# Kernel optimization log

Measured on AMD Instinct MI355X. Metric: run time of the kernel, lower is better.

The kernel has to match this reference:

```python
import jax, jax.numpy as jnp
import numpy as np

EMB = 768

def _mlp2(x, Wa, Wb):
    # relu(LL2(relu(LL1(x)))), bias-free linears stored as [out, in]
    return jax.nn.relu(jax.nn.relu(x @ Wa.T) @ Wb.T)

def setup_inputs() -> dict:
    key = jax.random.key(0)
    ks = jax.random.split(key, 6)
    n, m = 16, 4096  # maxlen = 64 paragraphs -> 64*64 pair slots
    X_data = jax.random.normal(ks[0], (n, 1 + m, 3 * EMB), dtype=jnp.float32)
    # first token carries num_clusters metadata (unused by the differentiable path)
    W1 = jax.random.normal(ks[1], (256, EMB), dtype=jnp.float32) * 0.02
    W2 = jax.random.normal(ks[2], (128, 256), dtype=jnp.float32) * 0.02
    W3 = jax.random.normal(ks[3], (256, EMB), dtype=jnp.float32) * 0.02
    W4 = jax.random.normal(ks[4], (128, 256), dtype=jnp.float32) * 0.02
    W5 = jax.random.normal(ks[5], (1, 128), dtype=jnp.float32) * 0.02
    return {"X_data": X_data, "W1": W1, "W2": W2, "W3": W3, "W4": W4, "W5": W5}

def reference(X_data, W1, W2, W3, W4, W5):
    # CATSCluster differentiable path: QueryScaler on X_data[:, 1:, :]
    X = X_data[:, 1:, :]                      # [n, m, 3*EMB]
    Xq = X[..., :EMB]
    Xp1 = X[..., EMB:2 * EMB]
    Xp2 = X[..., 2 * EMB:]
    Xp1z = _mlp2(Xp1, W1, W2)                 # [n, m, 128]
    Xp2z = _mlp2(Xp2, W1, W2)
    Xqz = _mlp2(Xq, W3, W4)
    Xpqz = Xqz * jnp.abs(Xp1z - Xp2z)         # [n, m, 128]
    dist = jnp.tanh(jax.nn.relu(Xpqz @ W5.T))[..., 0]  # [n, m]
    n, m = dist.shape
    p = int(np.sqrt(m))                       # maxlen
    # batch_pairscore_matrix fed to the host-side clustering step
    return dist.reshape(n, p, p)
```

## Files before the change

kernel.cpp:

```cpp
#include <hip/hip_runtime.h>
#include <hip/hip_bf16.h>


typedef short short8 __attribute__((ext_vector_type(8)));
typedef float f32x4 __attribute__((ext_vector_type(4)));

#define W1H_OFF 0u
#define W1L_OFF 196608u
#define W3H_OFF 393216u
#define W3L_OFF 589824u
#define W2H_OFF 786432u
#define W2L_OFF 819200u
#define W4H_OFF 851968u
#define W4L_OFF 884736u

__device__ __forceinline__ unsigned short bf16_rne(float f) {
  unsigned int u = __float_as_uint(f);
  u += 0x7FFFu + ((u >> 16) & 1u);
  return (unsigned short)(u >> 16);
}

__device__ __forceinline__ void split_bf16(float f, unsigned short& h, unsigned short& l) {
  h = bf16_rne(f);
  float fh = __uint_as_float(((unsigned int)h) << 16);
  l = bf16_rne(f - fh);
}

__global__ __launch_bounds__(256) void prep_weights(
    const float* __restrict__ W1, const float* __restrict__ W2,
    const float* __restrict__ W3, const float* __restrict__ W4,
    unsigned short* __restrict__ ws)
{
  int i = blockIdx.x * 256 + threadIdx.x;
  if (i < 196608) {
    unsigned short h, l;
    split_bf16(W1[i], h, l); ws[W1H_OFF + i] = h; ws[W1L_OFF + i] = l;
    split_bf16(W3[i], h, l); ws[W3H_OFF + i] = h; ws[W3L_OFF + i] = l;
    if (i < 32768) {
      split_bf16(W2[i], h, l); ws[W2H_OFF + i] = h; ws[W2L_OFF + i] = l;
      split_bf16(W4[i], h, l); ws[W4H_OFF + i] = h; ws[W4L_OFF + i] = l;
    }
  }
}

#define STRIDE_A 40
#define STRIDE_H 264

__global__ __launch_bounds__(256) void catsc_main(
    const float* __restrict__ X, const unsigned short* __restrict__ ws,
    const float* __restrict__ W5, float* __restrict__ out)
{
  __shared__ short lsA[2][2][64 * STRIDE_A];
  __shared__ short lsH[64 * STRIDE_H];
  __shared__ float lsPart[4][64];

  const int tid  = threadIdx.x;
  const int wave = tid >> 6;
  const int lane = tid & 63;
  const int l15  = lane & 15;
  const int q    = lane >> 4;
  const int blk  = blockIdx.x;

  const float* Xb = X + (size_t)((blk >> 6) * 4097 + 1 + ((blk & 63) << 6)) * 2304;

  const int srow = tid >> 3;
  const int f4   = (tid & 7) << 2;

  f32x4 z[3][4][2];

#pragma unroll
  for (int s = 0; s < 3; ++s) {
    const unsigned short* B1h = ws + (s == 0 ? W3H_OFF : W1H_OFF);
    const unsigned short* B1l = ws + (s == 0 ? W3L_OFF : W1L_OFF);
    const unsigned short* B2h = ws + (s == 0 ? W4H_OFF : W2H_OFF);
    const unsigned short* B2l = ws + (s == 0 ? W4L_OFF : W2L_OFF);
    const int so = s * 768;

    f32x4 acc[4][4];
#pragma unroll
    for (int m = 0; m < 4; ++m)
#pragma unroll
      for (int n = 0; n < 4; ++n)
        acc[m][n] = f32x4{0.f, 0.f, 0.f, 0.f};

#pragma unroll
    for (int it = 0; it < 2; ++it) {
      int rr = srow + 32 * it;
      float4 v = *(const float4*)(Xb + (size_t)rr * 2304 + so + f4);
      unsigned short h0,h1,h2,h3,l0,l1,l2,l3;
      split_bf16(v.x,h0,l0); split_bf16(v.y,h1,l1);
      split_bf16(v.z,h2,l2); split_bf16(v.w,h3,l3);
      uint2 ph, pl;
      ph.x = (unsigned)h0 | ((unsigned)h1 << 16); ph.y = (unsigned)h2 | ((unsigned)h3 << 16);
      pl.x = (unsigned)l0 | ((unsigned)l1 << 16); pl.y = (unsigned)l2 | ((unsigned)l3 << 16);
      *(uint2*)&lsA[0][0][rr * STRIDE_A + f4] = ph;
      *(uint2*)&lsA[0][1][rr * STRIDE_A + f4] = pl;
    }
    __syncthreads();

    for (int c = 0; c < 24; ++c) {
      const int b = c & 1;
      if (c + 1 < 24) {
        const int nb = b ^ 1;
#pragma unroll
        for (int it = 0; it < 2; ++it) {
          int rr = srow + 32 * it;
          float4 v = *(const float4*)(Xb + (size_t)rr * 2304 + so + (c + 1) * 32 + f4);
          unsigned short h0,h1,h2,h3,l0,l1,l2,l3;
          split_bf16(v.x,h0,l0); split_bf16(v.y,h1,l1);
          split_bf16(v.z,h2,l2); split_bf16(v.w,h3,l3);
          uint2 ph, pl;
          ph.x = (unsigned)h0 | ((unsigned)h1 << 16); ph.y = (unsigned)h2 | ((unsigned)h3 << 16);
          pl.x = (unsigned)l0 | ((unsigned)l1 << 16); pl.y = (unsigned)l2 | ((unsigned)l3 << 16);
          *(uint2*)&lsA[nb][0][rr * STRIDE_A + f4] = ph;
          *(uint2*)&lsA[nb][1][rr * STRIDE_A + f4] = pl;
        }
      }
      short8 Bh[4], Bl[4];
#pragma unroll
      for (int n = 0; n < 4; ++n) {
        size_t off = (size_t)((wave * 4 + n) * 16 + l15) * 768 + c * 32 + q * 8;
        Bh[n] = *(const short8*)(B1h + off);
        Bl[n] = *(const short8*)(B1l + off);
      }
      short8 Ah[4], Al[4];
#pragma unroll
      for (int m = 0; m < 4; ++m) {
        int a = (m * 16 + l15) * STRIDE_A + q * 8;
        Ah[m] = *(const short8*)&lsA[b][0][a];
        Al[m] = *(const short8*)&lsA[b][1][a];
      }
#pragma unroll
      for (int m = 0; m < 4; ++m)
#pragma unroll
        for (int n = 0; n < 4; ++n)
          acc[m][n] = __builtin_amdgcn_mfma_f32_16x16x32_bf16(Ah[m], Bh[n], acc[m][n], 0, 0, 0);
#pragma unroll
      for (int m = 0; m < 4; ++m)
#pragma unroll
        for (int n = 0; n < 4; ++n)
          acc[m][n] = __builtin_amdgcn_mfma_f32_16x16x32_bf16(Ah[m], Bl[n], acc[m][n], 0, 0, 0);
#pragma unroll
      for (int m = 0; m < 4; ++m)
#pragma unroll
        for (int n = 0; n < 4; ++n)
          acc[m][n] = __builtin_amdgcn_mfma_f32_16x16x32_bf16(Al[m], Bh[n], acc[m][n], 0, 0, 0);
      __syncthreads();
    }

#pragma unroll
    for (int m = 0; m < 4; ++m)
#pragma unroll
      for (int n = 0; n < 4; ++n) {
        int col = (wave * 4 + n) * 16 + l15;
#pragma unroll
        for (int i = 0; i < 4; ++i) {
          int row = m * 16 + q * 4 + i;
          lsH[row * STRIDE_H + col] = bf16_rne(fmaxf(acc[m][n][i], 0.f));
        }
      }
    __syncthreads();

    f32x4 acc2[4][2];
#pragma unroll
    for (int m = 0; m < 4; ++m)
#pragma unroll
      for (int n = 0; n < 2; ++n)
        acc2[m][n] = f32x4{0.f, 0.f, 0.f, 0.f};

    for (int c2 = 0; c2 < 8; ++c2) {
      short8 Ch[2], Cl[2];
#pragma unroll
      for (int n2 = 0; n2 < 2; ++n2) {
        size_t off = (size_t)((wave * 2 + n2) * 16 + l15) * 256 + c2 * 32 + q * 8;
        Ch[n2] = *(const short8*)(B2h + off);
        Cl[n2] = *(const short8*)(B2l + off);
      }
      short8 Ha[4];
#pragma unroll
      for (int m = 0; m < 4; ++m)
        Ha[m] = *(const short8*)&lsH[(m * 16 + l15) * STRIDE_H + c2 * 32 + q * 8];
#pragma unroll
      for (int m = 0; m < 4; ++m)
#pragma unroll
        for (int n2 = 0; n2 < 2; ++n2)
          acc2[m][n2] = __builtin_amdgcn_mfma_f32_16x16x32_bf16(Ha[m], Ch[n2], acc2[m][n2], 0, 0, 0);
#pragma unroll
      for (int m = 0; m < 4; ++m)
#pragma unroll
        for (int n2 = 0; n2 < 2; ++n2)
          acc2[m][n2] = __builtin_amdgcn_mfma_f32_16x16x32_bf16(Ha[m], Cl[n2], acc2[m][n2], 0, 0, 0);
    }
#pragma unroll
    for (int m = 0; m < 4; ++m)
#pragma unroll
      for (int n2 = 0; n2 < 2; ++n2)
#pragma unroll
        for (int i = 0; i < 4; ++i)
          z[s][m][n2][i] = fmaxf(acc2[m][n2][i], 0.f);
  }

  const float w5c0 = W5[(wave * 2 + 0) * 16 + l15];
  const float w5c1 = W5[(wave * 2 + 1) * 16 + l15];
#pragma unroll
  for (int m = 0; m < 4; ++m) {
#pragma unroll
    for (int i = 0; i < 4; ++i) {
      float v = z[0][m][0][i] * fabsf(z[1][m][0][i] - z[2][m][0][i]) * w5c0
              + z[0][m][1][i] * fabsf(z[1][m][1][i] - z[2][m][1][i]) * w5c1;
      v += __shfl_xor(v, 1);
      v += __shfl_xor(v, 2);
      v += __shfl_xor(v, 4);
      v += __shfl_xor(v, 8);
      if (l15 == 0) lsPart[wave][m * 16 + q * 4 + i] = v;
    }
  }
  __syncthreads();
  if (tid < 64) {
    float sum = lsPart[0][tid] + lsPart[1][tid] + lsPart[2][tid] + lsPart[3][tid];
    out[(size_t)blk * 64 + tid] = tanhf(fmaxf(sum, 0.f));
  }
}

extern "C" void kernel_launch(void* const* d_in, const int* in_sizes, int n_in,
                              void* d_out, int out_size, void* d_ws, size_t ws_size,
                              hipStream_t stream) {
  const float* X  = (const float*)d_in[0];
  const float* W1 = (const float*)d_in[1];
  const float* W2 = (const float*)d_in[2];
  const float* W3 = (const float*)d_in[3];
  const float* W4 = (const float*)d_in[4];
  const float* W5 = (const float*)d_in[5];
  float* out = (float*)d_out;
  unsigned short* ws = (unsigned short*)d_ws;

  prep_weights<<<dim3(768), dim3(256), 0, stream>>>(W1, W2, W3, W4, ws);
  catsc_main<<<dim3(1024), dim3(256), 0, stream>>>(X, ws, W5, out);
}
```

Measured before the change: 1.208 ms.

## Use 512-thread blocks, fold branch epilogue incrementally, and prefetch X two chunks ahead

Doubles the block to 8 waves so each wave owns half as many output columns in both GEMM stages, cutting accumulator registers. The kernel no longer keeps all three branch outputs alive: it builds |z1 - z2| right after the second branch and then multiplies by the query branch and reduces. Global loads of X now run two chunks ahead in registers, so the fetch overlaps the MFMA work before the value is split and written to LDS. This trades per-wave MFMA density and extra barrier participants for higher occupancy and better latency hiding on the memory-bound X stream.

```diff
diff --git a/kernel.cpp b/kernel.cpp
--- a/kernel.cpp
+++ b/kernel.cpp
@@ -1,5 +1,4 @@
 #include <hip/hip_runtime.h>
-#include <hip/hip_bf16.h>
 
 
 typedef short short8 __attribute__((ext_vector_type(8)));
@@ -46,13 +45,13 @@
 #define STRIDE_A 40
 #define STRIDE_H 264
 
-__global__ __launch_bounds__(256) void catsc_main(
+__global__ __launch_bounds__(512, 4) void catsc_main(
     const float* __restrict__ X, const unsigned short* __restrict__ ws,
     const float* __restrict__ W5, float* __restrict__ out)
 {
   __shared__ short lsA[2][2][64 * STRIDE_A];
   __shared__ short lsH[64 * STRIDE_H];
-  __shared__ float lsPart[4][64];
+  __shared__ float lsPart[8][64];
 
   const int tid  = threadIdx.x;
   const int wave = tid >> 6;
@@ -66,60 +65,49 @@
   const int srow = tid >> 3;
   const int f4   = (tid & 7) << 2;
 
-  f32x4 z[3][4][2];
+  f32x4 zp[4];
 
 #pragma unroll
   for (int s = 0; s < 3; ++s) {
-    const unsigned short* B1h = ws + (s == 0 ? W3H_OFF : W1H_OFF);
-    const unsigned short* B1l = ws + (s == 0 ? W3L_OFF : W1L_OFF);
-    const unsigned short* B2h = ws + (s == 0 ? W4H_OFF : W2H_OFF);
-    const unsigned short* B2l = ws + (s == 0 ? W4L_OFF : W2L_OFF);
-    const int so = s * 768;
-
-    f32x4 acc[4][4];
+    const int so = (s == 0) ? 768 : (s == 1) ? 1536 : 0;
+    const unsigned short* B1h = ws + (s == 2 ? W3H_OFF : W1H_OFF);
+    const unsigned short* B1l = ws + (s == 2 ? W3L_OFF : W1L_OFF);
+    const unsigned short* B2h = ws + (s == 2 ? W4H_OFF : W2H_OFF);
+    const unsigned short* B2l = ws + (s == 2 ? W4L_OFF : W2L_OFF);
+
+    const float* Xrow = Xb + (size_t)srow * 2304 + so + f4;
+
+    f32x4 acc[4][2];
 #pragma unroll
     for (int m = 0; m < 4; ++m)
 #pragma unroll
-      for (int n = 0; n < 4; ++n)
+      for (int n = 0; n < 2; ++n)
         acc[m][n] = f32x4{0.f, 0.f, 0.f, 0.f};
 
-#pragma unroll
-    for (int it = 0; it < 2; ++it) {
-      int rr = srow + 32 * it;
-      float4 v = *(const float4*)(Xb + (size_t)rr * 2304 + so + f4);
+    {
+      float4 v0 = *(const float4*)(Xrow);
       unsigned short h0,h1,h2,h3,l0,l1,l2,l3;
-      split_bf16(v.x,h0,l0); split_bf16(v.y,h1,l1);
-      split_bf16(v.z,h2,l2); split_bf16(v.w,h3,l3);
+      split_bf16(v0.x,h0,l0); split_bf16(v0.y,h1,l1);
+      split_bf16(v0.z,h2,l2); split_bf16(v0.w,h3,l3);
       uint2 ph, pl;
       ph.x = (unsigned)h0 | ((unsigned)h1 << 16); ph.y = (unsigned)h2 | ((unsigned)h3 << 16);
       pl.x = (unsigned)l0 | ((unsigned)l1 << 16); pl.y = (unsigned)l2 | ((unsigned)l3 << 16);
-      *(uint2*)&lsA[0][0][rr * STRIDE_A + f4] = ph;
-      *(uint2*)&lsA[0][1][rr * STRIDE_A + f4] = pl;
-    }
+      *(uint2*)&lsA[0][0][srow * STRIDE_A + f4] = ph;
+      *(uint2*)&lsA[0][1][srow * STRIDE_A + f4] = pl;
+    }
+    float4 vB = *(const float4*)(Xrow + 32);
     __syncthreads();
 
     for (int c = 0; c < 24; ++c) {
       const int b = c & 1;
-      if (c + 1 < 24) {
-        const int nb = b ^ 1;
-#pragma unroll
-        for (int it = 0; it < 2; ++it) {
-          int rr = srow + 32 * it;
-          float4 v = *(const float4*)(Xb + (size_t)rr * 2304 + so + (c + 1) * 32 + f4);
-          unsigned short h0,h1,h2,h3,l0,l1,l2,l3;
-          split_bf16(v.x,h0,l0); split_bf16(v.y,h1,l1);
-          split_bf16(v.z,h2,l2); split_bf16(v.w,h3,l3);
-          uint2 ph, pl;
-          ph.x = (unsigned)h0 | ((unsigned)h1 << 16); ph.y = (unsigned)h2 | ((unsigned)h3 << 16);
-          pl.x = (unsigned)l0 | ((unsigned)l1 << 16); pl.y = (unsigned)l2 | ((unsigned)l3 << 16);
-          *(uint2*)&lsA[nb][0][rr * STRIDE_A + f4] = ph;
-          *(uint2*)&lsA[nb][1][rr * STRIDE_A + f4] = pl;
-        }
-      }
-      short8 Bh[4], Bl[4];
-#pragma unroll
-      for (int n = 0; n < 4; ++n) {
-        size_t off = (size_t)((wave * 4 + n) * 16 + l15) * 768 + c * 32 + q * 8;
+
+      const int cl = (c + 2 < 24) ? (c + 2) : 23;
+      float4 vN = *(const float4*)(Xrow + cl * 32);
+
+      short8 Bh[2], Bl[2];
+#pragma unroll
+      for (int n = 0; n < 2; ++n) {
+        size_t off = (size_t)((wave * 2 + n) * 16 + l15) * 768 + c * 32 + q * 8;
         Bh[n] = *(const short8*)(B1h + off);
         Bl[n] = *(const short8*)(B1l + off);
       }
@@ -130,29 +118,44 @@
         Ah[m] = *(const short8*)&lsA[b][0][a];
         Al[m] = *(const short8*)&lsA[b][1][a];
       }
-#pragma unroll
-      for (int m = 0; m < 4; ++m)
-#pragma unroll
-        for (int n = 0; n < 4; ++n)
+
+      if (c + 1 < 24) {
+        unsigned short h0,h1,h2,h3,l0,l1,l2,l3;
+        split_bf16(vB.x,h0,l0); split_bf16(vB.y,h1,l1);
+        split_bf16(vB.z,h2,l2); split_bf16(vB.w,h3,l3);
+        uint2 ph, pl;
+        ph.x = (unsigned)h0 | ((unsigned)h1 << 16); ph.y = (unsigned)h2 | ((unsigned)h3 << 16);
+        pl.x = (unsigned)l0 | ((unsigned)l1 << 16); pl.y = (unsigned)l2 | ((unsigned)l3 << 16);
+        const int wb = b ^ 1;
+        *(uint2*)&lsA[wb][0][srow * STRIDE_A + f4] = ph;
+        *(uint2*)&lsA[wb][1][srow * STRIDE_A + f4] = pl;
+      }
+
+#pragma unroll
+      for (int m = 0; m < 4; ++m)
+#pragma unroll
+        for (int n = 0; n < 2; ++n)
           acc[m][n] = __builtin_amdgcn_mfma_f32_16x16x32_bf16(Ah[m], Bh[n], acc[m][n], 0, 0, 0);
 #pragma unroll
       for (int m = 0; m < 4; ++m)
 #pragma unroll
-        for (int n = 0; n < 4; ++n)
+        for (int n = 0; n < 2; ++n)
           acc[m][n] = __builtin_amdgcn_mfma_f32_16x16x32_bf16(Ah[m], Bl[n], acc[m][n], 0, 0, 0);
 #pragma unroll
       for (int m = 0; m < 4; ++m)
 #pragma unroll
-        for (int n = 0; n < 4; ++n)
+        for (int n = 0; n < 2; ++n)
           acc[m][n] = __builtin_amdgcn_mfma_f32_16x16x32_bf16(Al[m], Bh[n], acc[m][n], 0, 0, 0);
+
       __syncthreads();
+      vB = vN;
     }
 
 #pragma unroll
     for (int m = 0; m < 4; ++m)
 #pragma unroll
-      for (int n = 0; n < 4; ++n) {
-        int col = (wave * 4 + n) * 16 + l15;
+      for (int n = 0; n < 2; ++n) {
+        int col = (wave * 2 + n) * 16 + l15;
 #pragma unroll
         for (int i = 0; i < 4; ++i) {
           int row = m * 16 + q * 4 + i;
@@ -161,63 +164,58 @@
       }
     __syncthreads();
 
-    f32x4 acc2[4][2];
-#pragma unroll
-    for (int m = 0; m < 4; ++m)
-#pragma unroll
-      for (int n = 0; n < 2; ++n)
-        acc2[m][n] = f32x4{0.f, 0.f, 0.f, 0.f};
+    f32x4 acc2[4];
+#pragma unroll
+    for (int m = 0; m < 4; ++m) acc2[m] = f32x4{0.f, 0.f, 0.f, 0.f};
 
     for (int c2 = 0; c2 < 8; ++c2) {
-      short8 Ch[2], Cl[2];
-#pragma unroll
-      for (int n2 = 0; n2 < 2; ++n2) {
-        size_t off = (size_t)((wave * 2 + n2) * 16 + l15) * 256 + c2 * 32 + q * 8;
-        Ch[n2] = *(const short8*)(B2h + off);
-        Cl[n2] = *(const short8*)(B2l + off);
-      }
+      size_t off = (size_t)(wave * 16 + l15) * 256 + c2 * 32 + q * 8;
+      short8 Ch = *(const short8*)(B2h + off);
+      short8 Cl = *(const short8*)(B2l + off);
       short8 Ha[4];
 #pragma unroll
       for (int m = 0; m < 4; ++m)
         Ha[m] = *(const short8*)&lsH[(m * 16 + l15) * STRIDE_H + c2 * 32 + q * 8];
 #pragma unroll
       for (int m = 0; m < 4; ++m)
-#pragma unroll
-        for (int n2 = 0; n2 < 2; ++n2)
-          acc2[m][n2] = __builtin_amdgcn_mfma_f32_16x16x32_bf16(Ha[m], Ch[n2], acc2[m][n2], 0, 0, 0);
-#pragma unroll
-      for (int m = 0; m < 4; ++m)
-#pragma unroll
-        for (int n2 = 0; n2 < 2; ++n2)
-          acc2[m][n2] = __builtin_amdgcn_mfma_f32_16x16x32_bf16(Ha[m], Cl[n2], acc2[m][n2], 0, 0, 0);
-    }
-#pragma unroll
-    for (int m = 0; m < 4; ++m)
-#pragma unroll
-      for (int n2 = 0; n2 < 2; ++n2)
+        acc2[m] = __builtin_amdgcn_mfma_f32_16x16x32_bf16(Ha[m], Ch, acc2[m], 0, 0, 0);
+#pragma unroll
+      for (int m = 0; m < 4; ++m)
+        acc2[m] = __builtin_amdgcn_mfma_f32_16x16x32_bf16(Ha[m], Cl, acc2[m], 0, 0, 0);
+    }
+
+    if (s == 0) {
+#pragma unroll
+      for (int m = 0; m < 4; ++m)
 #pragma unroll
         for (int i = 0; i < 4; ++i)
-          z[s][m][n2][i] = fmaxf(acc2[m][n2][i], 0.f);
+          zp[m][i] = fmaxf(acc2[m][i], 0.f);
+    } else if (s == 1) {
+#pragma unroll
+      for (int m = 0; m < 4; ++m)
+#pragma unroll
+        for (int i = 0; i < 4; ++i)
+          zp[m][i] = fabsf(zp[m][i] - fmaxf(acc2[m][i], 0.f));
+    } else {
+      const float w5c = W5[wave * 16 + l15];
+#pragma unroll
+      for (int m = 0; m < 4; ++m)
+#pragma unroll
+        for (int i = 0; i < 4; ++i) {
+          float v = fmaxf(acc2[m][i], 0.f) * zp[m][i] * w5c;
+          v += __shfl_xor(v, 1);
+          v += __shfl_xor(v, 2);
+          v += __shfl_xor(v, 4);
+          v += __shfl_xor(v, 8);
+          if (l15 == 0) lsPart[wave][m * 16 + q * 4 + i] = v;
+        }
+    }
   }
 
-  const float w5c0 = W5[(wave * 2 + 0) * 16 + l15];
-  const float w5c1 = W5[(wave * 2 + 1) * 16 + l15];
-#pragma unroll
-  for (int m = 0; m < 4; ++m) {
-#pragma unroll
-    for (int i = 0; i < 4; ++i) {
-      float v = z[0][m][0][i] * fabsf(z[1][m][0][i] - z[2][m][0][i]) * w5c0
-              + z[0][m][1][i] * fabsf(z[1][m][1][i] - z[2][m][1][i]) * w5c1;
-      v += __shfl_xor(v, 1);
-      v += __shfl_xor(v, 2);
-      v += __shfl_xor(v, 4);
-      v += __shfl_xor(v, 8);
-      if (l15 == 0) lsPart[wave][m * 16 + q * 4 + i] = v;
-    }
-  }
   __syncthreads();
   if (tid < 64) {
-    float sum = lsPart[0][tid] + lsPart[1][tid] + lsPart[2][tid] + lsPart[3][tid];
+    float sum = lsPart[0][tid] + lsPart[1][tid] + lsPart[2][tid] + lsPart[3][tid]
+              + lsPart[4][tid] + lsPart[5][tid] + lsPart[6][tid] + lsPart[7][tid];
     out[(size_t)blk * 64 + tid] = tanhf(fmaxf(sum, 0.f));
   }
 }
@@ -235,5 +233,5 @@
   unsigned short* ws = (unsigned short*)d_ws;
 
   prep_weights<<<dim3(768), dim3(256), 0, stream>>>(W1, W2, W3, W4, ws);
-  catsc_main<<<dim3(1024), dim3(256), 0, stream>>>(X, ws, W5, out);
-}
+  catsc_main<<<dim3(1024), dim3(512), 0, stream>>>(X, ws, W5, out);
+}
```

After: 1.090 ms. 1.11x faster.
